# Optimization experiments

Hardware: AMD Instinct MI355X
Metric: run time of the kernel (lower is better)

## Reference

```python
import jax, jax.numpy as jnp
import numpy as np
import math

N = 50000      # nodes
E = 800000     # edges
D = 128        # in/out channels (hidden_dim)
H = 16         # heads
C = D // H     # per-head channels = 8
DH = 4 * D     # mlp hidden = 512
EPS = 1e-5


def layernorm(x, g, b):
    mu = jnp.mean(x, axis=-1, keepdims=True)
    var = jnp.var(x, axis=-1, keepdims=True)
    return (x - mu) * jax.lax.rsqrt(var + EPS) * g + b


def setup_inputs() -> dict:
    key = jax.random.key(0)
    ks = jax.random.split(key, 16)
    s = lambda k, shape, fan: jax.random.normal(k, shape, jnp.float32) / np.sqrt(fan)
    inp = {
        "x": jax.random.normal(ks[0], (N, D), jnp.float32),
        "edge_index": jax.random.randint(ks[1], (2, E), 0, N, jnp.int32),
        "edge_attr": jax.random.normal(ks[2], (E, D), jnp.float32),
        # layer norm 1
        "ln1_g": jnp.ones((D,), jnp.float32), "ln1_b": jnp.zeros((D,), jnp.float32),
        # q/k/v/self projections (in=D, out=H*C=D)
        "wq": s(ks[3], (D, D), D), "bq": jnp.zeros((D,), jnp.float32),
        "wk": s(ks[4], (D, D), D), "bk": jnp.zeros((D,), jnp.float32),
        "wv": s(ks[5], (D, D), D), "bv": jnp.zeros((D,), jnp.float32),
        "ws": s(ks[6], (D, D), D), "bs": jnp.zeros((D,), jnp.float32),
        # edge projection (edge_dim=D -> H*C)
        "we": s(ks[7], (D, D), D), "be": jnp.zeros((D,), jnp.float32),
        # output projection
        "wp": s(ks[8], (D, D), D), "bp": jnp.zeros((D,), jnp.float32),
        # node_dst_mlp: LN -> Linear(D,4D) -> SiLU -> Linear(4D,D)
        "mlp_ln_g": jnp.ones((D,), jnp.float32), "mlp_ln_b": jnp.zeros((D,), jnp.float32),
        "w1": s(ks[9], (D, DH), D), "b1": jnp.zeros((DH,), jnp.float32),
        "w2": s(ks[10], (DH, D), DH), "b2": jnp.zeros((D,), jnp.float32),
    }
    return inp


def reference(x, edge_index, edge_attr, ln1_g, ln1_b, wq, bq, wk, bk, wv, bv,
              ws, bs, we, be, wp, bp, mlp_ln_g, mlp_ln_b, w1, b1, w2, b2):
    src, dst = edge_index[0], edge_index[1]  # message j -> i

    h = layernorm(x, ln1_g, ln1_b)
    q = (h @ wq + bq).reshape(N, H, C)
    k = (h @ wk + bk).reshape(N, H, C)
    v = (h @ wv + bv).reshape(N, H, C)
    x_r = h @ ws + bs                         # [N, D]

    # per-edge gather + edge-feature add
    k_j = k[src] + (edge_attr @ we + be).reshape(E, H, C)  # [E,H,C]
    alpha = jnp.sum(q[dst] * k_j, axis=-1) / math.sqrt(C)  # [E,H]

    # segment softmax over destination nodes
    m = jax.ops.segment_max(alpha, dst, num_segments=N)    # [N,H]
    ex = jnp.exp(alpha - m[dst])
    denom = jax.ops.segment_sum(ex, dst, num_segments=N)   # [N,H]
    alpha = ex / denom[dst]

    # weighted scatter-add aggregation
    msg = v[src] * alpha[..., None]                        # [E,H,C]
    agg = jax.ops.segment_sum(msg, dst, num_segments=N).reshape(N, D)

    out = (agg + x_r) @ wp + bp
    out = out + x                                          # residual to raw input
    mlp_out = jax.nn.silu(layernorm(out, mlp_ln_g, mlp_ln_b) @ w1 + b1) @ w2 + b2
    return mlp_out + out
```

## Files before the change

kernel.cpp:

```cpp
#include <hip/hip_runtime.h>

#define N_NODES 50000
#define N_EDGES 800000
#define D 128
#define H 16
#define DH 512

typedef __attribute__((ext_vector_type(8))) short short8;
typedef __attribute__((ext_vector_type(4))) float f32x4;

static __device__ __forceinline__ unsigned short f2bf(float f) {
    unsigned u = __float_as_uint(f);
    u += 0x7FFF + ((u >> 16) & 1);
    return (unsigned short)(u >> 16);
}
static __device__ __forceinline__ float bf2f(unsigned short u) {
    return __uint_as_float(((unsigned)u) << 16);
}

__global__ void ln_kernel(const float* __restrict__ x, const float* __restrict__ g,
                          const float* __restrict__ b, unsigned short* __restrict__ out, int n) {
    int w = (blockIdx.x * blockDim.x + threadIdx.x) >> 6;
    int lane = threadIdx.x & 63;
    if (w >= n) return;
    float2 v = *(const float2*)(x + (size_t)w * D + lane * 2);
    float s = v.x + v.y, ss = v.x * v.x + v.y * v.y;
#pragma unroll
    for (int off = 32; off; off >>= 1) { s += __shfl_xor(s, off); ss += __shfl_xor(ss, off); }
    float mean = s * (1.0f / D);
    float var = ss * (1.0f / D) - mean * mean;
    float rstd = rsqrtf(var + 1e-5f);
    float2 gv = *(const float2*)(g + lane * 2);
    float2 bv = *(const float2*)(b + lane * 2);
    ushort2 o;
    o.x = f2bf((v.x - mean) * rstd * gv.x + bv.x);
    o.y = f2bf((v.y - mean) * rstd * gv.y + bv.y);
    *(ushort2*)(out + (size_t)w * D + lane * 2) = o;
}

__global__ void prep_kernel(const float* __restrict__ wq, const float* __restrict__ wk,
                            const float* __restrict__ wv, const float* __restrict__ ws,
                            const float* __restrict__ we, const float* __restrict__ wp,
                            const float* __restrict__ w1, const float* __restrict__ w2,
                            const float* __restrict__ bq, const float* __restrict__ bk,
                            const float* __restrict__ bv, const float* __restrict__ bs,
                            unsigned short* __restrict__ wqkvsT, unsigned short* __restrict__ weT,
                            unsigned short* __restrict__ wpT, unsigned short* __restrict__ w1T,
                            unsigned short* __restrict__ w2T, float* __restrict__ bias_qkvs) {
    int idx = blockIdx.x * blockDim.x + threadIdx.x;
    if (idx < 65536) {
        int seg = idx >> 14, r = idx & 16383;
        const float* src = seg == 0 ? wq : seg == 1 ? wk : seg == 2 ? wv : ws;
        int o = r >> 7, i = r & 127;
        wqkvsT[idx] = f2bf(src[i * 128 + o]);
    } else if (idx < 81920) {
        int r = idx - 65536; int o = r >> 7, i = r & 127;
        weT[r] = f2bf(we[i * 128 + o]);
    } else if (idx < 98304) {
        int r = idx - 81920; int o = r >> 7, i = r & 127;
        wpT[r] = f2bf(wp[i * 128 + o]);
    } else if (idx < 163840) {
        int r = idx - 98304; int o = r >> 7, i = r & 127;
        w1T[r] = f2bf(w1[i * 512 + o]);
    } else if (idx < 229376) {
        int r = idx - 163840; int o = r >> 9, i = r & 511;
        w2T[r] = f2bf(w2[i * 128 + o]);
    } else if (idx < 229888) {
        int r = idx - 229376;
        const float* p = r < 128 ? bq : r < 256 ? bk : r < 384 ? bv : bs;
        bias_qkvs[r] = p[r & 127];
    }
}

__global__ void hist_kernel(const int* __restrict__ edge_index, int* __restrict__ counts) {
    int e = blockIdx.x * blockDim.x + threadIdx.x;
    if (e < N_EDGES) atomicAdd(&counts[edge_index[N_EDGES + e]], 1);
}

__global__ void scan1_kernel(const int* __restrict__ counts, int* __restrict__ excl,
                             int* __restrict__ bsum) {
    __shared__ int sm[1024];
    int b = blockIdx.x, tid = threadIdx.x;
    int idx = b * 1024 + tid;
    int v = (idx < N_NODES) ? counts[idx] : 0;
    sm[tid] = v;
    __syncthreads();
    for (int off = 1; off < 1024; off <<= 1) {
        int t = (tid >= off) ? sm[tid - off] : 0;
        __syncthreads();
        sm[tid] += t;
        __syncthreads();
    }
    if (idx < N_NODES) excl[idx] = sm[tid] - v;
    if (tid == 1023) bsum[b] = sm[1023];
}

__global__ void scan2_kernel(int* __restrict__ bsum, int nb) {
    if (threadIdx.x == 0 && blockIdx.x == 0) {
        int run = 0;
        for (int i = 0; i < nb; ++i) { int v = bsum[i]; bsum[i] = run; run += v; }
    }
}

__global__ void scan3_kernel(const int* __restrict__ excl, const int* __restrict__ bsum,
                             int* __restrict__ row_ptr, int* __restrict__ cursor) {
    int b = blockIdx.x, tid = threadIdx.x;
    int idx = b * 1024 + tid;
    if (idx < N_NODES) {
        int v = bsum[b] + excl[idx];
        row_ptr[idx] = v;
        cursor[idx] = v;
    }
    if (idx == 0) row_ptr[N_NODES] = N_EDGES;
}

__global__ void scatter_kernel(const int* __restrict__ edge_index, int* __restrict__ cursor,
                               int* __restrict__ slot_of, int* __restrict__ src_ord) {
    int e = blockIdx.x * blockDim.x + threadIdx.x;
    if (e < N_EDGES) {
        int dst = edge_index[N_EDGES + e];
        int pos = atomicAdd(&cursor[dst], 1);
        slot_of[e] = pos;
        src_ord[pos] = edge_index[e];
    }
}

enum { EPI_F32 = 0, EPI_RESID = 1, EPI_SILU_BF = 2, EPI_ADDOUT = 3, EPI_BF16 = 4, EPI_QKVS = 5 };

template <int KD, int EPI>
__global__ void gemm_kernel(const unsigned short* __restrict__ A, const unsigned short* __restrict__ BT,
                            const float* __restrict__ bias, void* __restrict__ outp,
                            const float* __restrict__ extra, int M, int Nout) {
    int wave = threadIdx.x >> 6, lane = threadIdx.x & 63;
    int lr = lane & 15, lq = lane >> 4;
    int row0 = (blockIdx.x * 4 + wave) * 16;
    int col0 = blockIdx.y * 64;
    int arow = row0 + lr;
    if (arow >= M) arow = M - 1;
    f32x4 z = {0.f, 0.f, 0.f, 0.f};
    f32x4 acc[4] = {z, z, z, z};
#pragma unroll
    for (int t = 0; t < KD / 32; ++t) {
        short8 a = *(const short8*)(A + (size_t)arow * KD + t * 32 + lq * 8);
#pragma unroll
        for (int cf = 0; cf < 4; ++cf) {
            short8 b = *(const short8*)(BT + (size_t)(col0 + cf * 16 + lr) * KD + t * 32 + lq * 8);
            acc[cf] = __builtin_amdgcn_mfma_f32_16x16x32_bf16(a, b, acc[cf], 0, 0, 0);
        }
    }
#pragma unroll
    for (int cf = 0; cf < 4; ++cf) {
        int col = col0 + cf * 16 + lr;
        float bv = bias[col];
#pragma unroll
        for (int r = 0; r < 4; ++r) {
            int row = row0 + lq * 4 + r;
            if (row >= M) continue;
            float v = acc[cf][r] + bv;
            if (EPI == EPI_F32) {
                ((float*)outp)[(size_t)row * Nout + col] = v;
            } else if (EPI == EPI_RESID) {
                ((float*)outp)[(size_t)row * Nout + col] = v + extra[(size_t)row * D + col];
            } else if (EPI == EPI_SILU_BF) {
                float sg = 1.0f / (1.0f + __expf(-v));
                ((unsigned short*)outp)[(size_t)row * Nout + col] = f2bf(v * sg);
            } else if (EPI == EPI_ADDOUT) {
                ((float*)outp)[(size_t)row * Nout + col] = v + extra[(size_t)row * D + col];
            } else if (EPI == EPI_QKVS) {
                int seg = col >> 7, c = col & 127;
                size_t o = (seg == 0) ? (size_t)c : (seg == 1) ? (size_t)(128 + 2 * c)
                         : (seg == 2) ? (size_t)(129 + 2 * c) : (size_t)(384 + c);
                ((unsigned short*)outp)[(size_t)row * 512 + o] = f2bf(v);
            } else {
                ((unsigned short*)outp)[(size_t)row * Nout + col] = f2bf(v);
            }
        }
    }
}

#define ES_GRID 3584
__global__ __launch_bounds__(128)
void edge_score_kernel(const float* __restrict__ edge_attr,
                       const unsigned short* __restrict__ weT,
                       const float* __restrict__ be, const int* __restrict__ edge_index,
                       const int* __restrict__ slot_of,
                       const unsigned short* __restrict__ qkvs,
                       unsigned short* __restrict__ qE16) {
    __shared__ unsigned short q_lds[32][132];
    __shared__ float s_lds[32][20];
    const int NTILE = N_EDGES / 32;
    int wave = threadIdx.x >> 6, lane = threadIdx.x & 63;
    int lr = lane & 15, lq = lane >> 4;
    int w16 = wave * 16;
    int plane = lane >> 5, h2 = lane & 31;

    for (int tile = blockIdx.x; tile < NTILE; tile += ES_GRID) {
        int e0w = tile * 32 + w16;

        f32x4 lo[4], hi[4];
#pragma unroll
        for (int t = 0; t < 4; ++t) {
            const f32x4* p = (const f32x4*)(edge_attr + (size_t)(e0w + lr) * D + t * 32 + lq * 8);
            lo[t] = __builtin_nontemporal_load(p);
            hi[t] = __builtin_nontemporal_load(p + 1);
        }

        int dstv = edge_index[N_EDGES + e0w + lr];
        int slotv = slot_of[e0w + lr];
        ushort4 qreg[8];
#pragma unroll
        for (int it = 0; it < 8; ++it) {
            int dst = __shfl(dstv, it * 2 + plane);
            qreg[it] = *(const ushort4*)(qkvs + (size_t)dst * 512 + h2 * 4);
        }

        short8 a[4];
#pragma unroll
        for (int t = 0; t < 4; ++t) {
            short8 av;
            av[0] = f2bf(lo[t][0]); av[1] = f2bf(lo[t][1]); av[2] = f2bf(lo[t][2]); av[3] = f2bf(lo[t][3]);
            av[4] = f2bf(hi[t][0]); av[5] = f2bf(hi[t][1]); av[6] = f2bf(hi[t][2]); av[7] = f2bf(hi[t][3]);
            a[t] = av;
        }

#pragma unroll
        for (int it = 0; it < 8; ++it)
            *(ushort4*)(&q_lds[w16 + it * 2 + plane][h2 * 4]) = qreg[it];

        f32x4 z = {0.f, 0.f, 0.f, 0.f};
        f32x4 acc[8] = {z, z, z, z, z, z, z, z};
#pragma unroll
        for (int cf = 0; cf < 8; ++cf) {
#pragma unroll
            for (int t = 0; t < 4; ++t) {
                short8 b = *(const short8*)(weT + (size_t)(cf * 16 + lr) * D + t * 32 + lq * 8);
                acc[cf] = __builtin_amdgcn_mfma_f32_16x16x32_bf16(b, a[t], acc[cf], 0, 0, 0);
            }
        }

#pragma unroll
        for (int cf = 0; cf < 8; ++cf) {
            int ch = cf * 16 + lq * 4;
            ushort4 q4 = *(const ushort4*)(&q_lds[w16 + lr][ch]);
            f32x4 be4 = *(const f32x4*)(be + ch);
            float p = bf2f(q4.x) * (acc[cf][0] + be4[0])
                    + bf2f(q4.y) * (acc[cf][1] + be4[1])
                    + bf2f(q4.z) * (acc[cf][2] + be4[2])
                    + bf2f(q4.w) * (acc[cf][3] + be4[3]);
            p += __shfl_xor(p, 16);
            if ((lq & 1) == 0)
                s_lds[w16 + lr][cf * 2 + (lq >> 1)] = p;
        }

        int el16 = lane >> 2;
        int slot = __shfl(slotv, el16);
        f32x4 sv = *(const f32x4*)(&s_lds[w16 + el16][(lane & 3) * 4]);
        ushort4 o;
        o.x = f2bf(sv[0]); o.y = f2bf(sv[1]); o.z = f2bf(sv[2]); o.w = f2bf(sv[3]);
        *(ushort4*)(qE16 + (size_t)slot * 16 + (lane & 3) * 4) = o;
    }
}

#define AGG_GRID 2048
__global__ void agg_kernel(const int* __restrict__ row_ptr, const int* __restrict__ src_ord,
                           const unsigned short* __restrict__ qE16, const unsigned short* __restrict__ qkvs,
                           unsigned short* __restrict__ aggxr) {
    int lane = threadIdx.x & 63;
    int c = lane * 2, h = lane >> 2;
    const float scale = 0.35355339059327373f;
    int nw = (AGG_GRID * 256) >> 6;
    for (int w = (int)((blockIdx.x * blockDim.x + threadIdx.x) >> 6); w < N_NODES; w += nw) {
        int s = row_ptr[w], e = row_ptr[w + 1], deg = e - s;
        int src_p = (lane < deg) ? src_ord[s + lane] : 0;
        ushort2 q2 = *(const ushort2*)(qkvs + (size_t)w * 512 + c);
        float qa = bf2f(q2.x), qb = bf2f(q2.y);
        float acc0 = 0.f, acc1 = 0.f, den = 0.f;
        for (int i = 0; i < deg; ++i) {
            int src = (i < 64) ? __shfl(src_p, i) : src_ord[s + i];
            ushort4 kv = *(const ushort4*)(qkvs + (size_t)src * 512 + 128 + (size_t)c * 2);
            float pa = qa * bf2f(kv.x) + qb * bf2f(kv.z);
            pa += __shfl_xor(pa, 1);
            pa += __shfl_xor(pa, 2);
            float qEv = bf2f(qE16[(size_t)(s + i) * 16 + h]);
            float ex = __expf((pa + qEv) * scale);
            acc0 += ex * bf2f(kv.y);
            acc1 += ex * bf2f(kv.w);
            den += ex;
        }
        float inv = den > 0.f ? 1.0f / den : 0.f;
        ushort2 x2 = *(const ushort2*)(qkvs + (size_t)w * 512 + 384 + c);
        ushort2 o;
        o.x = f2bf(acc0 * inv + bf2f(x2.x));
        o.y = f2bf(acc1 * inv + bf2f(x2.y));
        *(ushort2*)(aggxr + (size_t)w * D + c) = o;
    }
}

extern "C" void kernel_launch(void* const* d_in, const int* in_sizes, int n_in,
                              void* d_out, int out_size, void* d_ws, size_t ws_size,
                              hipStream_t stream) {
    const float* x = (const float*)d_in[0];
    const int* edge_index = (const int*)d_in[1];
    const float* edge_attr = (const float*)d_in[2];
    const float* ln1_g = (const float*)d_in[3];
    const float* ln1_b = (const float*)d_in[4];
    const float* wq = (const float*)d_in[5];  const float* bq = (const float*)d_in[6];
    const float* wk = (const float*)d_in[7];  const float* bk = (const float*)d_in[8];
    const float* wv = (const float*)d_in[9];  const float* bv = (const float*)d_in[10];
    const float* wsw = (const float*)d_in[11]; const float* bs = (const float*)d_in[12];
    const float* we = (const float*)d_in[13]; const float* be = (const float*)d_in[14];
    const float* wp = (const float*)d_in[15]; const float* bp = (const float*)d_in[16];
    const float* mlp_g = (const float*)d_in[17]; const float* mlp_b = (const float*)d_in[18];
    const float* w1 = (const float*)d_in[19]; const float* b1 = (const float*)d_in[20];
    const float* w2 = (const float*)d_in[21]; const float* b2 = (const float*)d_in[22];

    char* base = (char*)d_ws;
    size_t off = 0;
    auto alloc = [&](size_t bytes) -> char* {
        char* p = base + off;
        off = (off + bytes + 255) & ~(size_t)255;
        return p;
    };
    unsigned short* qkvs   = (unsigned short*)alloc((size_t)N_NODES * 512 * 2);
    unsigned short* qE16   = (unsigned short*)alloc((size_t)N_EDGES * H * 2);
    unsigned short* h_bf   = (unsigned short*)alloc((size_t)N_NODES * D * 2);
    unsigned short* aggxr  = (unsigned short*)alloc((size_t)N_NODES * D * 2);
    float* outbuf          = (float*)alloc((size_t)N_NODES * D * 4);
    unsigned short* ln2_bf = (unsigned short*)alloc((size_t)N_NODES * D * 2);
    unsigned short* silu_bf= (unsigned short*)alloc((size_t)N_NODES * DH * 2);
    int* counts            = (int*)alloc((size_t)N_NODES * 4);
    int* row_ptr           = (int*)alloc((size_t)(N_NODES + 1) * 4);
    int* cursor            = (int*)alloc((size_t)N_NODES * 4);
    int* slot_of           = (int*)alloc((size_t)N_EDGES * 4);
    int* src_ord           = (int*)alloc((size_t)N_EDGES * 4);
    int* excl              = (int*)alloc((size_t)N_NODES * 4);
    int* bsum              = (int*)alloc(64 * 4);
    unsigned short* wqkvsT = (unsigned short*)alloc(512 * 128 * 2);
    unsigned short* weT    = (unsigned short*)alloc(128 * 128 * 2);
    unsigned short* wpT    = (unsigned short*)alloc(128 * 128 * 2);
    unsigned short* w1T    = (unsigned short*)alloc(512 * 128 * 2);
    unsigned short* w2T    = (unsigned short*)alloc(128 * 512 * 2);
    float* bias_qkvs       = (float*)alloc(512 * 4);

    const int NB = (N_NODES + 1023) / 1024;

    prep_kernel<<<898, 256, 0, stream>>>(wq, wk, wv, wsw, we, wp, w1, w2, bq, bk, bv, bs,
                                         wqkvsT, weT, wpT, w1T, w2T, bias_qkvs);

    (void)hipMemsetAsync(counts, 0, (size_t)N_NODES * 4, stream);
    hist_kernel<<<(N_EDGES + 255) / 256, 256, 0, stream>>>(edge_index, counts);
    scan1_kernel<<<NB, 1024, 0, stream>>>(counts, excl, bsum);
    scan2_kernel<<<1, 64, 0, stream>>>(bsum, NB);
    scan3_kernel<<<NB, 1024, 0, stream>>>(excl, bsum, row_ptr, cursor);
    scatter_kernel<<<(N_EDGES + 255) / 256, 256, 0, stream>>>(edge_index, cursor, slot_of, src_ord);

    ln_kernel<<<(N_NODES + 3) / 4, 256, 0, stream>>>(x, ln1_g, ln1_b, h_bf, N_NODES);

    dim3 g_node((N_NODES + 63) / 64, 8);
    gemm_kernel<128, EPI_QKVS><<<g_node, 256, 0, stream>>>(h_bf, wqkvsT, bias_qkvs, qkvs, nullptr, N_NODES, 512);

    edge_score_kernel<<<ES_GRID, 128, 0, stream>>>(edge_attr, weT, be, edge_index, slot_of, qkvs, qE16);

    agg_kernel<<<AGG_GRID, 256, 0, stream>>>(row_ptr, src_ord, qE16, qkvs, aggxr);

    dim3 g_out((N_NODES + 63) / 64, 2);
    gemm_kernel<128, EPI_RESID><<<g_out, 256, 0, stream>>>(aggxr, wpT, bp, outbuf, x, N_NODES, 128);

    ln_kernel<<<(N_NODES + 3) / 4, 256, 0, stream>>>(outbuf, mlp_g, mlp_b, ln2_bf, N_NODES);

    dim3 g_mlp1((N_NODES + 63) / 64, 8);
    gemm_kernel<128, EPI_SILU_BF><<<g_mlp1, 256, 0, stream>>>(ln2_bf, w1T, b1, silu_bf, nullptr, N_NODES, 512);

    dim3 g_mlp2((N_NODES + 63) / 64, 2);
    gemm_kernel<512, EPI_ADDOUT><<<g_mlp2, 256, 0, stream>>>(silu_bf, w2T, b2, (float*)d_out, outbuf, N_NODES, 128);
}
```

Baseline: 615.4 us.

## Software-pipeline edge_score tiles with register prefetch over contiguous chunks

```diff
diff --git a/kernel.cpp b/kernel.cpp
--- a/kernel.cpp
+++ b/kernel.cpp
@@ -178,7 +178,9 @@
     }
 }
 
-#define ES_GRID 3584
+#define ES_CHUNK 7
+#define ES_NTILE (N_EDGES / 32)
+#define ES_GRID ((ES_NTILE + ES_CHUNK - 1) / ES_CHUNK)
 __global__ __launch_bounds__(128)
 void edge_score_kernel(const float* __restrict__ edge_attr,
                        const unsigned short* __restrict__ weT,
@@ -188,44 +190,74 @@
                        unsigned short* __restrict__ qE16) {
     __shared__ unsigned short q_lds[32][132];
     __shared__ float s_lds[32][20];
-    const int NTILE = N_EDGES / 32;
     int wave = threadIdx.x >> 6, lane = threadIdx.x & 63;
     int lr = lane & 15, lq = lane >> 4;
     int w16 = wave * 16;
     int plane = lane >> 5, h2 = lane & 31;
 
-    for (int tile = blockIdx.x; tile < NTILE; tile += ES_GRID) {
-        int e0w = tile * 32 + w16;
-
-        f32x4 lo[4], hi[4];
-#pragma unroll
-        for (int t = 0; t < 4; ++t) {
-            const f32x4* p = (const f32x4*)(edge_attr + (size_t)(e0w + lr) * D + t * 32 + lq * 8);
-            lo[t] = __builtin_nontemporal_load(p);
-            hi[t] = __builtin_nontemporal_load(p + 1);
-        }
-
-        int dstv = edge_index[N_EDGES + e0w + lr];
-        int slotv = slot_of[e0w + lr];
-        ushort4 qreg[8];
-#pragma unroll
-        for (int it = 0; it < 8; ++it) {
-            int dst = __shfl(dstv, it * 2 + plane);
-            qreg[it] = *(const ushort4*)(qkvs + (size_t)dst * 512 + h2 * 4);
-        }
-
-        short8 a[4];
-#pragma unroll
-        for (int t = 0; t < 4; ++t) {
-            short8 av;
-            av[0] = f2bf(lo[t][0]); av[1] = f2bf(lo[t][1]); av[2] = f2bf(lo[t][2]); av[3] = f2bf(lo[t][3]);
-            av[4] = f2bf(hi[t][0]); av[5] = f2bf(hi[t][1]); av[6] = f2bf(hi[t][2]); av[7] = f2bf(hi[t][3]);
-            a[t] = av;
-        }
-
+    int t0 = blockIdx.x * ES_CHUNK;
+    if (t0 >= ES_NTILE) return;
+    int tend = min(t0 + ES_CHUNK, ES_NTILE);
+
+    int e0w = t0 * 32 + w16;
+    f32x4 attrf[8];
+#pragma unroll
+    for (int t = 0; t < 4; ++t) {
+        const f32x4* p = (const f32x4*)(edge_attr + (size_t)(e0w + lr) * D + t * 32 + lq * 8);
+        attrf[2 * t]     = __builtin_nontemporal_load(p);
+        attrf[2 * t + 1] = __builtin_nontemporal_load(p + 1);
+    }
+    int dstv = edge_index[N_EDGES + e0w + lr];
+    int slotv = slot_of[e0w + lr];
+    ushort4 qreg[8];
+#pragma unroll
+    for (int it = 0; it < 8; ++it) {
+        int dst = __shfl(dstv, it * 2 + plane);
+        qreg[it] = *(const ushort4*)(qkvs + (size_t)dst * 512 + h2 * 4);
+    }
+    int dstv_n = 0, slotv_n = 0;
+    if (t0 + 1 < tend) {
+        int e1w = (t0 + 1) * 32 + w16;
+        dstv_n = edge_index[N_EDGES + e1w + lr];
+        slotv_n = slot_of[e1w + lr];
+    }
+
+    for (int tile = t0; tile < tend; ++tile) {
 #pragma unroll
         for (int it = 0; it < 8; ++it)
             *(ushort4*)(&q_lds[w16 + it * 2 + plane][h2 * 4]) = qreg[it];
+
+        short8 a[4];
+#pragma unroll
+        for (int t = 0; t < 4; ++t) {
+            f32x4 lo = attrf[2 * t], hi = attrf[2 * t + 1];
+            short8 av;
+            av[0] = f2bf(lo[0]); av[1] = f2bf(lo[1]); av[2] = f2bf(lo[2]); av[3] = f2bf(lo[3]);
+            av[4] = f2bf(hi[0]); av[5] = f2bf(hi[1]); av[6] = f2bf(hi[2]); av[7] = f2bf(hi[3]);
+            a[t] = av;
+        }
+        int slot_cur = slotv;
+
+        if (tile + 1 < tend) {
+            int e1w = (tile + 1) * 32 + w16;
+#pragma unroll
+            for (int t = 0; t < 4; ++t) {
+                const f32x4* p = (const f32x4*)(edge_attr + (size_t)(e1w + lr) * D + t * 32 + lq * 8);
+                attrf[2 * t]     = __builtin_nontemporal_load(p);
+                attrf[2 * t + 1] = __builtin_nontemporal_load(p + 1);
+            }
+#pragma unroll
+            for (int it = 0; it < 8; ++it) {
+                int dst = __shfl(dstv_n, it * 2 + plane);
+                qreg[it] = *(const ushort4*)(qkvs + (size_t)dst * 512 + h2 * 4);
+            }
+        }
+        dstv = dstv_n; slotv = slotv_n;
+        if (tile + 2 < tend) {
+            int e2w = (tile + 2) * 32 + w16;
+            dstv_n = edge_index[N_EDGES + e2w + lr];
+            slotv_n = slot_of[e2w + lr];
+        }
 
         f32x4 z = {0.f, 0.f, 0.f, 0.f};
         f32x4 acc[8] = {z, z, z, z, z, z, z, z};
@@ -253,7 +285,7 @@
         }
 
         int el16 = lane >> 2;
-        int slot = __shfl(slotv, el16);
+        int slot = __shfl(slot_cur, el16);
         f32x4 sv = *(const f32x4*)(&s_lds[w16 + el16][(lane & 3) * 4]);
         ushort4 o;
         o.x = f2bf(sv[0]); o.y = f2bf(sv[1]); o.z = f2bf(sv[2]); o.w = f2bf(sv[3]);
```

New measurement: 583.8 us, median of 2. 1.05x faster.

## Software-pipeline edge score kernel with double-buffered register prefetch over fixed chunks

Applied to the files above, without the earlier changes.

```diff
diff --git a/kernel.cpp b/kernel.cpp
--- a/kernel.cpp
+++ b/kernel.cpp
@@ -178,7 +178,76 @@
     }
 }
 
-#define ES_GRID 3584
+#define ES_CHUNK 8
+#define ES_NTILE (N_EDGES / 32)
+#define ES_GRID (ES_NTILE / ES_CHUNK)
+
+#define ES_LOAD(ATTR, QREG, J)                                                           \
+    do {                                                                                 \
+        int e0w_ = (t0 + (J)) * 32 + w16;                                                \
+        _Pragma("unroll")                                                                \
+        for (int t_ = 0; t_ < 4; ++t_) {                                                 \
+            const f32x4* p_ = (const f32x4*)(edge_attr + (size_t)(e0w_ + lr) * D + t_ * 32 + lq * 8); \
+            ATTR[2 * t_]     = __builtin_nontemporal_load(p_);                           \
+            ATTR[2 * t_ + 1] = __builtin_nontemporal_load(p_ + 1);                       \
+        }                                                                                \
+        int dsrc_ = ((J) < 4) ? dstP0 : dstP1;                                           \
+        _Pragma("unroll")                                                                \
+        for (int it_ = 0; it_ < 8; ++it_) {                                              \
+            int dst_ = __shfl(dsrc_, (((J) & 3) << 4) + it_ * 2 + plane);                \
+            QREG[it_] = *(const ushort4*)(qkvs + (size_t)dst_ * 512 + h2 * 4);           \
+        }                                                                                \
+    } while (0)
+
+#define ES_COMPUTE(ATTR, QREG, J, PF)                                                    \
+    do {                                                                                 \
+        _Pragma("unroll")                                                                \
+        for (int it_ = 0; it_ < 8; ++it_)                                                \
+            *(ushort4*)(&q_lds[w16 + it_ * 2 + plane][h2 * 4]) = QREG[it_];              \
+        short8 a_[4];                                                                    \
+        _Pragma("unroll")                                                                \
+        for (int t_ = 0; t_ < 4; ++t_) {                                                 \
+            f32x4 lo_ = ATTR[2 * t_], hi_ = ATTR[2 * t_ + 1];                            \
+            short8 av_;                                                                  \
+            av_[0] = f2bf(lo_[0]); av_[1] = f2bf(lo_[1]);                                \
+            av_[2] = f2bf(lo_[2]); av_[3] = f2bf(lo_[3]);                                \
+            av_[4] = f2bf(hi_[0]); av_[5] = f2bf(hi_[1]);                                \
+            av_[6] = f2bf(hi_[2]); av_[7] = f2bf(hi_[3]);                                \
+            a_[t_] = av_;                                                                \
+        }                                                                                \
+        PF;                                                                              \
+        f32x4 z_ = {0.f, 0.f, 0.f, 0.f};                                                 \
+        f32x4 acc_[8] = {z_, z_, z_, z_, z_, z_, z_, z_};                                \
+        _Pragma("unroll")                                                                \
+        for (int cf_ = 0; cf_ < 8; ++cf_) {                                              \
+            _Pragma("unroll")                                                            \
+            for (int t_ = 0; t_ < 4; ++t_) {                                             \
+                short8 b_ = *(const short8*)(weT + (size_t)(cf_ * 16 + lr) * D + t_ * 32 + lq * 8); \
+                acc_[cf_] = __builtin_amdgcn_mfma_f32_16x16x32_bf16(b_, a_[t_], acc_[cf_], 0, 0, 0); \
+            }                                                                            \
+        }                                                                                \
+        _Pragma("unroll")                                                                \
+        for (int cf_ = 0; cf_ < 8; ++cf_) {                                              \
+            int ch_ = cf_ * 16 + lq * 4;                                                 \
+            ushort4 q4_ = *(const ushort4*)(&q_lds[w16 + lr][ch_]);                      \
+            f32x4 be4_ = *(const f32x4*)(be + ch_);                                      \
+            float p_ = bf2f(q4_.x) * (acc_[cf_][0] + be4_[0])                            \
+                     + bf2f(q4_.y) * (acc_[cf_][1] + be4_[1])                            \
+                     + bf2f(q4_.z) * (acc_[cf_][2] + be4_[2])                            \
+                     + bf2f(q4_.w) * (acc_[cf_][3] + be4_[3]);                           \
+            p_ += __shfl_xor(p_, 16);                                                    \
+            if ((lq & 1) == 0)                                                           \
+                s_lds[w16 + lr][cf_ * 2 + (lq >> 1)] = p_;                               \
+        }                                                                                \
+        int ssrc_ = ((J) < 4) ? slotP0 : slotP1;                                         \
+        int el16_ = lane >> 2;                                                           \
+        int slot_ = __shfl(ssrc_, (((J) & 3) << 4) + el16_);                             \
+        f32x4 sv_ = *(const f32x4*)(&s_lds[w16 + el16_][(lane & 3) * 4]);                \
+        ushort4 o_;                                                                      \
+        o_.x = f2bf(sv_[0]); o_.y = f2bf(sv_[1]); o_.z = f2bf(sv_[2]); o_.w = f2bf(sv_[3]); \
+        *(ushort4*)(qE16 + (size_t)slot_ * 16 + (lane & 3) * 4) = o_;                    \
+    } while (0)
+
 __global__ __launch_bounds__(128)
 void edge_score_kernel(const float* __restrict__ edge_attr,
                        const unsigned short* __restrict__ weT,
@@ -188,77 +257,31 @@
                        unsigned short* __restrict__ qE16) {
     __shared__ unsigned short q_lds[32][132];
     __shared__ float s_lds[32][20];
-    const int NTILE = N_EDGES / 32;
     int wave = threadIdx.x >> 6, lane = threadIdx.x & 63;
     int lr = lane & 15, lq = lane >> 4;
     int w16 = wave * 16;
     int plane = lane >> 5, h2 = lane & 31;
-
-    for (int tile = blockIdx.x; tile < NTILE; tile += ES_GRID) {
-        int e0w = tile * 32 + w16;
-
-        f32x4 lo[4], hi[4];
-#pragma unroll
-        for (int t = 0; t < 4; ++t) {
-            const f32x4* p = (const f32x4*)(edge_attr + (size_t)(e0w + lr) * D + t * 32 + lq * 8);
-            lo[t] = __builtin_nontemporal_load(p);
-            hi[t] = __builtin_nontemporal_load(p + 1);
-        }
-
-        int dstv = edge_index[N_EDGES + e0w + lr];
-        int slotv = slot_of[e0w + lr];
-        ushort4 qreg[8];
-#pragma unroll
-        for (int it = 0; it < 8; ++it) {
-            int dst = __shfl(dstv, it * 2 + plane);
-            qreg[it] = *(const ushort4*)(qkvs + (size_t)dst * 512 + h2 * 4);
-        }
-
-        short8 a[4];
-#pragma unroll
-        for (int t = 0; t < 4; ++t) {
-            short8 av;
-            av[0] = f2bf(lo[t][0]); av[1] = f2bf(lo[t][1]); av[2] = f2bf(lo[t][2]); av[3] = f2bf(lo[t][3]);
-            av[4] = f2bf(hi[t][0]); av[5] = f2bf(hi[t][1]); av[6] = f2bf(hi[t][2]); av[7] = f2bf(hi[t][3]);
-            a[t] = av;
-        }
-
-#pragma unroll
-        for (int it = 0; it < 8; ++it)
-            *(ushort4*)(&q_lds[w16 + it * 2 + plane][h2 * 4]) = qreg[it];
-
-        f32x4 z = {0.f, 0.f, 0.f, 0.f};
-        f32x4 acc[8] = {z, z, z, z, z, z, z, z};
-#pragma unroll
-        for (int cf = 0; cf < 8; ++cf) {
-#pragma unroll
-            for (int t = 0; t < 4; ++t) {
-                short8 b = *(const short8*)(weT + (size_t)(cf * 16 + lr) * D + t * 32 + lq * 8);
-                acc[cf] = __builtin_amdgcn_mfma_f32_16x16x32_bf16(b, a[t], acc[cf], 0, 0, 0);
-            }
-        }
-
-#pragma unroll
-        for (int cf = 0; cf < 8; ++cf) {
-            int ch = cf * 16 + lq * 4;
-            ushort4 q4 = *(const ushort4*)(&q_lds[w16 + lr][ch]);
-            f32x4 be4 = *(const f32x4*)(be + ch);
-            float p = bf2f(q4.x) * (acc[cf][0] + be4[0])
-                    + bf2f(q4.y) * (acc[cf][1] + be4[1])
-                    + bf2f(q4.z) * (acc[cf][2] + be4[2])
-                    + bf2f(q4.w) * (acc[cf][3] + be4[3]);
-            p += __shfl_xor(p, 16);
-            if ((lq & 1) == 0)
-                s_lds[w16 + lr][cf * 2 + (lq >> 1)] = p;
-        }
-
-        int el16 = lane >> 2;
-        int slot = __shfl(slotv, el16);
-        f32x4 sv = *(const f32x4*)(&s_lds[w16 + el16][(lane & 3) * 4]);
-        ushort4 o;
-        o.x = f2bf(sv[0]); o.y = f2bf(sv[1]); o.z = f2bf(sv[2]); o.w = f2bf(sv[3]);
-        *(ushort4*)(qE16 + (size_t)slot * 16 + (lane & 3) * 4) = o;
-    }
+    int t0 = blockIdx.x * ES_CHUNK;
+
+    int tg = lane >> 4, te = lane & 15;
+    int dstP0 = edge_index[N_EDGES + (t0 + tg) * 32 + w16 + te];
+    int slotP0 = slot_of[(t0 + tg) * 32 + w16 + te];
+    int dstP1 = edge_index[N_EDGES + (t0 + 4 + tg) * 32 + w16 + te];
+    int slotP1 = slot_of[(t0 + 4 + tg) * 32 + w16 + te];
+
+    f32x4 attrA[8], attrB[8];
+    ushort4 qregA[8], qregB[8];
+    ES_LOAD(attrA, qregA, 0);
+    ES_LOAD(attrB, qregB, 1);
+
+    ES_COMPUTE(attrA, qregA, 0, ES_LOAD(attrA, qregA, 2));
+    ES_COMPUTE(attrB, qregB, 1, ES_LOAD(attrB, qregB, 3));
+    ES_COMPUTE(attrA, qregA, 2, ES_LOAD(attrA, qregA, 4));
+    ES_COMPUTE(attrB, qregB, 3, ES_LOAD(attrB, qregB, 5));
+    ES_COMPUTE(attrA, qregA, 4, ES_LOAD(attrA, qregA, 6));
+    ES_COMPUTE(attrB, qregB, 5, ES_LOAD(attrB, qregB, 7));
+    ES_COMPUTE(attrA, qregA, 6, );
+    ES_COMPUTE(attrB, qregB, 7, );
 }
 
 #define AGG_GRID 2048
```

New measurement: 802.6 us. 1.3x slower.
